# Performance work log

Measured on AMD Instinct MI355X. Metric: run time of the kernel, lower is better.

Reference implementation:

```python
import jax, jax.numpy as jnp
import numpy as np

N_NODES = 100000
N_EDGES = 1600000
N_GRAPHS = 256
IN_C = 64
HID = 128
OUT = 128
BN_EPS = 1e-5


def setup_inputs() -> dict:
    key = jax.random.key(0)
    ks = jax.random.split(key, 24)
    x = jax.random.normal(ks[0], (N_NODES, IN_C), jnp.float32)
    edge_index = jax.random.randint(ks[1], (2, N_EDGES), 0, N_NODES, dtype=jnp.int64 if jax.config.jax_enable_x64 else jnp.int32)
    batch = jnp.sort(jax.random.randint(ks[2], (N_NODES,), 0, N_GRAPHS))

    def lin(k, i, o):
        return (jax.random.normal(k, (i, o), jnp.float32) / np.float32(np.sqrt(i)))

    d = {"x": x, "edge_index": edge_index, "batch": batch}
    in_dims = [IN_C, HID, HID]
    for l in range(3):
        d[f"w1_{l}"] = lin(ks[3 + 6 * l], in_dims[l], HID)
        d[f"b1_{l}"] = jnp.zeros((HID,), jnp.float32)
        d[f"w2_{l}"] = lin(ks[4 + 6 * l], HID, HID)
        d[f"b2_{l}"] = jnp.zeros((HID,), jnp.float32)
        d[f"gamma_{l}"] = jnp.ones((HID,), jnp.float32)
        d[f"beta_{l}"] = jnp.zeros((HID,), jnp.float32)
    d["proj_w"] = lin(ks[22], HID, OUT)
    d["proj_b"] = jnp.zeros((OUT,), jnp.float32)
    return d


def _gin_forward(x, edge_index, batch, layers, proj_w, proj_b):
    src, dst = edge_index[0], edge_index[1]
    h = x
    for (w1, b1, w2, b2, g, b) in layers:
        # GINConv (eps=0, aggr='add'): MLP(h_i + sum_{j->i} h_j)
        agg = jax.ops.segment_sum(h[src], dst, num_segments=h.shape[0])
        z = h + agg
        z = jax.nn.relu(z @ w1 + b1) @ w2 + b2
        # BatchNorm1d, training mode (biased batch stats)
        mean = z.mean(axis=0)
        var = z.var(axis=0)
        z = (z - mean) * jax.lax.rsqrt(var + BN_EPS) * g + b
        h = jax.nn.relu(z)
    # global_mean_pool over graph ids
    s = jax.ops.segment_sum(h, batch, num_segments=N_GRAPHS)
    cnt = jax.ops.segment_sum(jnp.ones((h.shape[0], 1), h.dtype), batch, num_segments=N_GRAPHS)
    hg = s / jnp.maximum(cnt, 1.0)
    return hg @ proj_w + proj_b


def reference(x, edge_index, batch,
              w1_0, b1_0, w2_0, b2_0, gamma_0, beta_0,
              w1_1, b1_1, w2_1, b2_1, gamma_1, beta_1,
              w1_2, b1_2, w2_2, b2_2, gamma_2, beta_2,
              proj_w, proj_b):
    layers = [
        (w1_0, b1_0, w2_0, b2_0, gamma_0, beta_0),
        (w1_1, b1_1, w2_1, b2_1, gamma_1, beta_1),
        (w1_2, b1_2, w2_2, b2_2, gamma_2, beta_2),
    ]
    return _gin_forward(x, edge_index, batch, layers, proj_w, proj_b)
```

## Files before the change

### kernel.cpp

```cpp
#include <hip/hip_runtime.h>

#define N_NODES 100000
#define N_EDGES 1600000
#define N_GRAPHS 256
#define HID 128
#define BN_EPS 1e-5f

#define NT 1563
#define EB 4096
#define RB 391
#define MBLK 391
#define PB 1564

typedef __bf16 bf16x8 __attribute__((ext_vector_type(8)));
typedef __bf16 bf16x4 __attribute__((ext_vector_type(4)));
typedef __bf16 bf16x2 __attribute__((ext_vector_type(2)));
typedef float f32x4 __attribute__((ext_vector_type(4)));

__global__ __launch_bounds__(256) void setup_kernel(
    const float* __restrict__ x, __bf16* __restrict__ xb,
    const float* __restrict__ wa, const float* __restrict__ wb,
    const float* __restrict__ wc, const float* __restrict__ wd,
    const float* __restrict__ we, const float* __restrict__ wf,
    __bf16* __restrict__ wt,
    const int* __restrict__ batch, int* __restrict__ counts,
    const int* __restrict__ ei, int* __restrict__ tcnt) {
  __shared__ int hist[NT];
  int b = blockIdx.x;
  if (b < 6250) {
    int idx = b * 256 + threadIdx.x;
    if (idx >= N_NODES * 16) return;
    f32x4 v = ((const f32x4*)x)[idx];
    bf16x4 o = {(__bf16)v[0], (__bf16)v[1], (__bf16)v[2], (__bf16)v[3]};
    ((bf16x4*)xb)[idx] = o;
  } else if (b < 6250 + 352) {
    int idx = (b - 6250) * 256 + threadIdx.x;
    if (idx >= 90112) return;
    const float* w;
    int K, local;
    if (idx < 8192) { w = wa; K = 64; local = idx; }
    else {
      int s = (idx - 8192) / 16384;
      local = (idx - 8192) - s * 16384;
      K = 128;
      w = (s == 0) ? wb : (s == 1) ? wc : (s == 2) ? wd : (s == 3) ? we : wf;
    }
    int n = local / K, k = local - n * K;
    wt[idx] = (__bf16)w[k * 128 + n];
  } else if (b < 6609) {
    int t = (b - 6602) * 256 + threadIdx.x;
    int r0 = t * 64;
    if (r0 >= N_NODES) return;
    int rend = min(r0 + 64, N_NODES);
    int curg = batch[r0], cnt = 0;
    for (int r = r0; r < rend; r++) {
      int g = batch[r];
      if (g != curg) {
        atomicAdd(&counts[curg], cnt);
        curg = g;
        cnt = 1;
      } else {
        cnt++;
      }
    }
    atomicAdd(&counts[curg], cnt);
  } else {
    int t = threadIdx.x;
    for (int i = t; i < NT; i += 256) hist[i] = 0;
    __syncthreads();
    int base = (b - 6609) * EB;
#pragma unroll 4
    for (int i = 0; i < EB / 256; i++) {
      int e = base + i * 256 + t;
      if (e < N_EDGES) atomicAdd(&hist[ei[N_EDGES + e] >> 6], 1);
    }
    __syncthreads();
    for (int i = t; i < NT; i += 256) {
      int h = hist[i];
      if (h) atomicAdd(&tcnt[i], h);
    }
  }
}

__global__ __launch_bounds__(256) void tile_scan_kernel(const int* __restrict__ tcnt,
                                                        int* __restrict__ tstart,
                                                        int* __restrict__ gcursor) {
  __shared__ int ps[256];
  int t = threadIdx.x;
  const int CH = (NT + 255) / 256;
  int lo = t * CH, hi = min(lo + CH, NT);
  int s = 0;
  for (int i = lo; i < hi; i++) s += tcnt[i];
  ps[t] = s;
  __syncthreads();
  for (int off = 1; off < 256; off <<= 1) {
    int v = ps[t];
    int u = (t >= off) ? ps[t - off] : 0;
    __syncthreads();
    ps[t] = v + u;
    __syncthreads();
  }
  int base = (t == 0) ? 0 : ps[t - 1];
  for (int i = lo; i < hi; i++) {
    tstart[i] = base;
    gcursor[i] = base;
    base += tcnt[i];
  }
  if (t == 0) tstart[NT] = N_EDGES;
}

__global__ __launch_bounds__(256) void reorder2_kernel(const int* __restrict__ ei,
                                                       int* __restrict__ gcursor,
                                                       int* __restrict__ epack) {
  __shared__ int hist[NT];
  int t = threadIdx.x;
  for (int i = t; i < NT; i += 256) hist[i] = 0;
  __syncthreads();
  int base = blockIdx.x * EB;
#pragma unroll 4
  for (int i = 0; i < EB / 256; i++) {
    int e = base + i * 256 + t;
    if (e < N_EDGES) atomicAdd(&hist[ei[N_EDGES + e] >> 6], 1);
  }
  __syncthreads();
  for (int i = t; i < NT; i += 256) {
    int h = hist[i];
    if (h) hist[i] = atomicAdd(&gcursor[i], h);
  }
  __syncthreads();
#pragma unroll 4
  for (int i = 0; i < EB / 256; i++) {
    int e = base + i * 256 + t;
    if (e < N_EDGES) {
      int d = ei[N_EDGES + e];
      int s = ei[e];
      int pos = atomicAdd(&hist[d >> 6], 1);
      epack[pos] = (s << 6) | (d & 63);
    }
  }
}

__global__ __launch_bounds__(256) void row_sort_kernel(const int* __restrict__ tstart,
                                                       const int* __restrict__ epack,
                                                       int* __restrict__ starts,
                                                       int* __restrict__ srcs) {
  __shared__ int cnt[64];
  __shared__ int rbase[65];
  __shared__ int rofs[64];
  int t = threadIdx.x, b = blockIdx.x;
  int ts = tstart[b], te = tstart[b + 1];
  if (t < 64) cnt[t] = 0;
  __syncthreads();
  for (int i = ts + t; i < te; i += 256) atomicAdd(&cnt[epack[i] & 63], 1);
  __syncthreads();
  if (t == 0) {
    int a = 0;
    for (int r = 0; r < 64; r++) { rbase[r] = a; a += cnt[r]; }
    rbase[64] = a;
  }
  __syncthreads();
  if (t < 64) rofs[t] = ts + rbase[t];
  if (t <= 64) {
    int gr = b * 64 + t;
    if (gr <= N_NODES) starts[gr] = ts + rbase[t];
  }
  __syncthreads();
  for (int i = ts + t; i < te; i += 256) {
    int p = epack[i];
    int pos = atomicAdd(&rofs[p & 63], 1);
    srcs[pos] = p >> 6;
  }
}

template <int C, bool BN>
__global__ __launch_bounds__(256) void gather_kernel(const __bf16* __restrict__ h,
                                                     const float* __restrict__ accum,
                                                     const float* __restrict__ gamma,
                                                     const float* __restrict__ beta,
                                                     const int* __restrict__ starts,
                                                     const int* __restrict__ srcs,
                                                     __bf16* __restrict__ z) {
  const int lane = threadIdx.x & 63;
  const int row = __builtin_amdgcn_readfirstlane(blockIdx.x * 4 + (threadIdx.x >> 6));
  const int e0 = starts[row], e1 = starts[row + 1];

  if constexpr (C == 128) {
    float a0 = 0.f, a1 = 0.f, b0 = 0.f, b1 = 0.f;
    if constexpr (BN) {
      const int c0 = lane * 2, c1 = c0 + 1;
      const float invN = 1.f / (float)N_NODES;
      float m0 = accum[c0] * invN, m1 = accum[c1] * invN;
      float v0 = accum[HID + c0] * invN - m0 * m0;
      float v1 = accum[HID + c1] * invN - m1 * m1;
      a0 = gamma[c0] * rsqrtf(v0 + BN_EPS);
      a1 = gamma[c1] * rsqrtf(v1 + BN_EPS);
      b0 = beta[c0] - m0 * a0;
      b1 = beta[c1] - m1 * a1;
    }
#define ACCBN(vv, ss)                                                  \
    do {                                                               \
      if constexpr (BN) {                                              \
        ss.x += fmaxf(fmaf(a0, (float)(vv)[0], b0), 0.f);              \
        ss.y += fmaxf(fmaf(a1, (float)(vv)[1], b1), 0.f);              \
      } else {                                                         \
        ss.x += (float)(vv)[0];                                        \
        ss.y += (float)(vv)[1];                                        \
      }                                                                \
    } while (0)
    float2 s0 = {0.f, 0.f}, s1 = {0.f, 0.f}, s2 = {0.f, 0.f}, s3 = {0.f, 0.f};
    float2 s4 = {0.f, 0.f}, s5 = {0.f, 0.f}, s6 = {0.f, 0.f}, s7 = {0.f, 0.f};
    int e = e0;
    for (; e + 7 < e1; e += 8) {
      int i0 = srcs[e];
      int i1 = srcs[e + 1];
      int i2 = srcs[e + 2];
      int i3 = srcs[e + 3];
      int i4 = srcs[e + 4];
      int i5 = srcs[e + 5];
      int i6 = srcs[e + 6];
      int i7 = srcs[e + 7];
      bf16x2 v0 = *(const bf16x2*)(h + (size_t)i0 * 128 + lane * 2);
      bf16x2 v1 = *(const bf16x2*)(h + (size_t)i1 * 128 + lane * 2);
      bf16x2 v2 = *(const bf16x2*)(h + (size_t)i2 * 128 + lane * 2);
      bf16x2 v3 = *(const bf16x2*)(h + (size_t)i3 * 128 + lane * 2);
      bf16x2 v4 = *(const bf16x2*)(h + (size_t)i4 * 128 + lane * 2);
      bf16x2 v5 = *(const bf16x2*)(h + (size_t)i5 * 128 + lane * 2);
      bf16x2 v6 = *(const bf16x2*)(h + (size_t)i6 * 128 + lane * 2);
      bf16x2 v7 = *(const bf16x2*)(h + (size_t)i7 * 128 + lane * 2);
      ACCBN(v0, s0);
      ACCBN(v1, s1);
      ACCBN(v2, s2);
      ACCBN(v3, s3);
      ACCBN(v4, s4);
      ACCBN(v5, s5);
      ACCBN(v6, s6);
      ACCBN(v7, s7);
    }
    for (; e + 3 < e1; e += 4) {
      int i0 = srcs[e];
      int i1 = srcs[e + 1];
      int i2 = srcs[e + 2];
      int i3 = srcs[e + 3];
      bf16x2 v0 = *(const bf16x2*)(h + (size_t)i0 * 128 + lane * 2);
      bf16x2 v1 = *(const bf16x2*)(h + (size_t)i1 * 128 + lane * 2);
      bf16x2 v2 = *(const bf16x2*)(h + (size_t)i2 * 128 + lane * 2);
      bf16x2 v3 = *(const bf16x2*)(h + (size_t)i3 * 128 + lane * 2);
      ACCBN(v0, s0);
      ACCBN(v1, s1);
      ACCBN(v2, s2);
      ACCBN(v3, s3);
    }
    for (; e < e1; e++) {
      int i0 = srcs[e];
      bf16x2 vv = *(const bf16x2*)(h + (size_t)i0 * 128 + lane * 2);
      ACCBN(vv, s0);
    }
    bf16x2 sv = *(const bf16x2*)(h + (size_t)row * 128 + lane * 2);
    ACCBN(sv, s0);
    float tx = ((s0.x + s1.x) + (s2.x + s3.x)) + ((s4.x + s5.x) + (s6.x + s7.x));
    float ty = ((s0.y + s1.y) + (s2.y + s3.y)) + ((s4.y + s5.y) + (s6.y + s7.y));
    bf16x2 o = {(__bf16)tx, (__bf16)ty};
    *(bf16x2*)(z + (size_t)row * 128 + lane * 2) = o;
#undef ACCBN
  } else {
    float s0 = 0.f, s1 = 0.f, s2 = 0.f, s3 = 0.f;
    float s4 = 0.f, s5 = 0.f, s6 = 0.f, s7 = 0.f;
    int e = e0;
    for (; e + 7 < e1; e += 8) {
      int i0 = srcs[e];
      int i1 = srcs[e + 1];
      int i2 = srcs[e + 2];
      int i3 = srcs[e + 3];
      int i4 = srcs[e + 4];
      int i5 = srcs[e + 5];
      int i6 = srcs[e + 6];
      int i7 = srcs[e + 7];
      s0 += (float)h[(size_t)i0 * 64 + lane];
      s1 += (float)h[(size_t)i1 * 64 + lane];
      s2 += (float)h[(size_t)i2 * 64 + lane];
      s3 += (float)h[(size_t)i3 * 64 + lane];
      s4 += (float)h[(size_t)i4 * 64 + lane];
      s5 += (float)h[(size_t)i5 * 64 + lane];
      s6 += (float)h[(size_t)i6 * 64 + lane];
      s7 += (float)h[(size_t)i7 * 64 + lane];
    }
    for (; e + 3 < e1; e += 4) {
      int i0 = srcs[e];
      int i1 = srcs[e + 1];
      int i2 = srcs[e + 2];
      int i3 = srcs[e + 3];
      s0 += (float)h[(size_t)i0 * 64 + lane];
      s1 += (float)h[(size_t)i1 * 64 + lane];
      s2 += (float)h[(size_t)i2 * 64 + lane];
      s3 += (float)h[(size_t)i3 * 64 + lane];
    }
    for (; e < e1; e++) {
      int i0 = srcs[e];
      s0 += (float)h[(size_t)i0 * 64 + lane];
    }
    s0 += (float)h[(size_t)row * 64 + lane];
    float tot = ((s0 + s1) + (s2 + s3)) + ((s4 + s5) + (s6 + s7));
    z[(size_t)row * 64 + lane] = (__bf16)tot;
  }
}

template <int CIN>
__global__ __launch_bounds__(256, 1) void mlp_kernel(
    const __bf16* __restrict__ z, const __bf16* __restrict__ w1t,
    const float* __restrict__ b1, const __bf16* __restrict__ w2t,
    const float* __restrict__ b2, __bf16* __restrict__ u,
    float* __restrict__ part) {
  constexpr int CINP = CIN + 8;
  constexpr int TS = HID + 8;
  __shared__ __align__(16) __bf16 w1s[128 * CINP];
  __shared__ __align__(16) __bf16 w2s[128 * TS];
  __shared__ __align__(16) __bf16 hsm[4 * 64 * TS];

  const int tid = threadIdx.x;

  for (int i = tid; i < 128 * (CIN / 8); i += 256) {
    int r = i / (CIN / 8), c = i - r * (CIN / 8);
    *(bf16x8*)(w1s + r * CINP + c * 8) = *(const bf16x8*)(w1t + r * CIN + c * 8);
  }
  for (int i = tid; i < 128 * 16; i += 256) {
    int r = i >> 4, c = i & 15;
    *(bf16x8*)(w2s + r * TS + c * 8) = *(const bf16x8*)(w2t + r * HID + c * 8);
  }
  __syncthreads();

  const int wid = tid >> 6;
  const int lane = tid & 63;
  const int l16 = lane & 15;
  const int quad = lane >> 4;
  const int wgid = blockIdx.x * 4 + wid;
  const int rowbase = wgid * 64;
  const int nvalid = min(64, N_NODES - rowbase);
  __bf16* sm = hsm + wid * 64 * TS;

  if (nvalid <= 0) {
    float2 z2 = {0.f, 0.f};
    *(float2*)(part + (size_t)wgid * 256 + lane * 2) = z2;
    *(float2*)(part + (size_t)wgid * 256 + HID + lane * 2) = z2;
    return;
  }

  const f32x4 zero4 = {0.f, 0.f, 0.f, 0.f};
  f32x4 acc[8][4];

  {
#pragma unroll
    for (int ct = 0; ct < 8; ct++)
#pragma unroll
      for (int m = 0; m < 4; m++) acc[ct][m] = zero4;
#pragma unroll
    for (int ks = 0; ks < CIN / 32; ks++) {
      bf16x8 af[4];
#pragma unroll
      for (int m = 0; m < 4; m++) {
        int row = min(rowbase + m * 16 + l16, N_NODES - 1);
        af[m] = *(const bf16x8*)(z + (size_t)row * CIN + ks * 32 + quad * 8);
      }
#pragma unroll
      for (int ct = 0; ct < 8; ct++) {
        bf16x8 bfr = *(const bf16x8*)(w1s + (ct * 16 + l16) * CINP + ks * 32 + quad * 8);
#pragma unroll
        for (int m = 0; m < 4; m++)
          acc[ct][m] = __builtin_amdgcn_mfma_f32_16x16x32_bf16(af[m], bfr, acc[ct][m], 0, 0, 0);
      }
    }
#pragma unroll
    for (int ct = 0; ct < 8; ct++) {
      int col = ct * 16 + l16;
      float bias = b1[col];
#pragma unroll
      for (int m = 0; m < 4; m++)
#pragma unroll
        for (int r = 0; r < 4; r++) {
          float v = acc[ct][m][r] + bias;
          sm[(m * 16 + quad * 4 + r) * TS + col] = (__bf16)(v > 0.f ? v : 0.f);
        }
    }
  }

  {
#pragma unroll
    for (int ct = 0; ct < 8; ct++)
#pragma unroll
      for (int m = 0; m < 4; m++) acc[ct][m] = zero4;
#pragma unroll
    for (int ks = 0; ks < HID / 32; ks++) {
      bf16x8 af[4];
#pragma unroll
      for (int m = 0; m < 4; m++)
        af[m] = *(const bf16x8*)(sm + (m * 16 + l16) * TS + ks * 32 + quad * 8);
#pragma unroll
      for (int ct = 0; ct < 8; ct++) {
        bf16x8 bfr = *(const bf16x8*)(w2s + (ct * 16 + l16) * TS + ks * 32 + quad * 8);
#pragma unroll
        for (int m = 0; m < 4; m++)
          acc[ct][m] = __builtin_amdgcn_mfma_f32_16x16x32_bf16(af[m], bfr, acc[ct][m], 0, 0, 0);
      }
    }
  }

#pragma unroll
  for (int ct = 0; ct < 8; ct++) {
    int col = ct * 16 + l16;
    float bias = b2[col];
#pragma unroll
    for (int m = 0; m < 4; m++)
#pragma unroll
      for (int r = 0; r < 4; r++)
        sm[(m * 16 + quad * 4 + r) * TS + col] = (__bf16)(acc[ct][m][r] + bias);
  }

  for (int f = lane; f < nvalid * 16; f += 64) {
    int r = f >> 4, c8 = f & 15;
    bf16x8 v = *(const bf16x8*)(sm + r * TS + c8 * 8);
    *(bf16x8*)(u + (size_t)(rowbase + r) * HID + c8 * 8) = v;
  }

  {
    float s0 = 0.f, q0 = 0.f, s1 = 0.f, q1 = 0.f;
    for (int r = 0; r < nvalid; r++) {
      bf16x2 v = *(const bf16x2*)(sm + r * TS + lane * 2);
      float f0 = (float)v[0], f1 = (float)v[1];
      s0 += f0; q0 += f0 * f0;
      s1 += f1; q1 += f1 * f1;
    }
    float2 sp = {s0, s1}, qp = {q0, q1};
    *(float2*)(part + (size_t)wgid * 256 + lane * 2) = sp;
    *(float2*)(part + (size_t)wgid * 256 + HID + lane * 2) = qp;
  }
}

__global__ __launch_bounds__(256) void reduce_part_kernel(const float* __restrict__ part,
                                                          float* __restrict__ accum) {
  int t = threadIdx.x;
  float s = 0.f;
  for (int r = blockIdx.x; r < PB; r += gridDim.x)
    s += part[(size_t)r * 256 + t];
  atomicAdd(&accum[t], s);
}

__global__ __launch_bounds__(128) void bn_apply_pool_kernel(const __bf16* __restrict__ u,
                                                            const float* __restrict__ accum,
                                                            const float* __restrict__ gamma,
                                                            const float* __restrict__ beta,
                                                            const int* __restrict__ batch,
                                                            float* __restrict__ pool) {
  int c = threadIdx.x;
  int r0 = blockIdx.x * 64;
  if (r0 >= N_NODES) return;
  int rend = min(r0 + 64, N_NODES);
  const float invN = 1.f / (float)N_NODES;
  float mean = accum[c] * invN;
  float var = accum[HID + c] * invN - mean * mean;
  float a = gamma[c] * rsqrtf(var + BN_EPS);
  float b = beta[c] - mean * a;
  float accv = 0.f;
  int curg = -1;
  for (int r = r0; r < rend; r++) {
    int g = batch[r];
    if (g != curg) {
      if (curg >= 0) atomicAdd(&pool[curg * HID + c], accv);
      curg = g;
      accv = 0.f;
    }
    float v = (float)u[(size_t)r * HID + c];
    v = v * a + b;
    accv += (v > 0.f ? v : 0.f);
  }
  if (curg >= 0) atomicAdd(&pool[curg * HID + c], accv);
}

__global__ __launch_bounds__(128) void pool_proj_kernel(const float* __restrict__ pool,
                                                        const int* __restrict__ counts,
                                                        const float* __restrict__ pw,
                                                        const float* __restrict__ pb,
                                                        float* __restrict__ out) {
  int g = blockIdx.x;
  int c = threadIdx.x;
  __shared__ float hg[HID];
  float cnt = (float)max(counts[g], 1);
  hg[c] = pool[g * HID + c] / cnt;
  __syncthreads();
  float acc = pb[c];
#pragma unroll 8
  for (int k = 0; k < HID; k++) acc += hg[k] * pw[k * HID + c];
  out[g * HID + c] = acc;
}

extern "C" void kernel_launch(void* const* d_in, const int* in_sizes, int n_in,
                              void* d_out, int out_size, void* d_ws, size_t ws_size,
                              hipStream_t stream) {
  (void)in_sizes; (void)n_in; (void)out_size; (void)ws_size;
  const float* x = (const float*)d_in[0];
  const int* ei = (const int*)d_in[1];
  const int* batch = (const int*)d_in[2];
  const float* w1[3] = {(const float*)d_in[3], (const float*)d_in[9], (const float*)d_in[15]};
  const float* b1[3] = {(const float*)d_in[4], (const float*)d_in[10], (const float*)d_in[16]};
  const float* w2[3] = {(const float*)d_in[5], (const float*)d_in[11], (const float*)d_in[17]};
  const float* b2[3] = {(const float*)d_in[6], (const float*)d_in[12], (const float*)d_in[18]};
  const float* gm[3] = {(const float*)d_in[7], (const float*)d_in[13], (const float*)d_in[19]};
  const float* bt[3] = {(const float*)d_in[8], (const float*)d_in[14], (const float*)d_in[20]};
  const float* pw = (const float*)d_in[21];
  const float* pb = (const float*)d_in[22];
  float* out = (float*)d_out;

  char* ws = (char*)d_ws;
  __bf16* bufA = (__bf16*)ws;        ws += (size_t)N_NODES * HID * 2;
  __bf16* bufB = (__bf16*)ws;        ws += (size_t)N_NODES * HID * 2;
  __bf16* bufC = (__bf16*)ws;        ws += (size_t)N_NODES * HID * 2;
  __bf16* z0 = (__bf16*)ws;          ws += (size_t)N_NODES * 64 * 2;
  __bf16* xb = (__bf16*)ws;          ws += (size_t)N_NODES * 64 * 2;
  int* srcs = (int*)ws;              ws += (size_t)N_EDGES * 4;
  int* epack = (int*)ws;             ws += (size_t)N_EDGES * 4;
  int* starts = (int*)ws;            ws += (size_t)(N_NODES + 1) * 4;
  int* tcnt = (int*)ws;              ws += NT * 4;
  int* tstart = (int*)ws;            ws += (NT + 1) * 4;
  int* gcursor = (int*)ws;           ws += NT * 4;
  ws = (char*)(((uintptr_t)ws + 63) & ~(uintptr_t)63);
  float* part = (float*)ws;          ws += (size_t)PB * 256 * 4;
  __bf16* wt_all = (__bf16*)ws;      ws += 90112 * 2;
  ws = (char*)(((uintptr_t)ws + 63) & ~(uintptr_t)63);
  float* accum = (float*)ws;         ws += 3 * 256 * 4;
  float* pool = (float*)ws;          ws += N_GRAPHS * HID * 4;
  int* counts = (int*)ws;            ws += N_GRAPHS * 4;

  __bf16* w1t0 = wt_all;
  __bf16* w2t0 = wt_all + 8192;
  __bf16* w1t1 = wt_all + 24576;
  __bf16* w2t1 = wt_all + 40960;
  __bf16* w1t2 = wt_all + 57344;
  __bf16* w2t2 = wt_all + 73728;

  float* acc0 = accum;
  float* acc1 = accum + 256;
  float* acc2 = accum + 512;

  const int gat_blocks = (N_NODES + 3) / 4;

  hipMemsetAsync(accum, 0, 3 * 256 * 4 + (size_t)N_GRAPHS * HID * 4 + N_GRAPHS * 4, stream);
  hipMemsetAsync(tcnt, 0, NT * 4, stream);

  setup_kernel<<<7000, 256, 0, stream>>>(x, xb, w1[0], w2[0], w1[1], w2[1],
                                         w1[2], w2[2], wt_all, batch, counts, ei, tcnt);

  tile_scan_kernel<<<1, 256, 0, stream>>>(tcnt, tstart, gcursor);
  reorder2_kernel<<<RB, 256, 0, stream>>>(ei, gcursor, epack);
  row_sort_kernel<<<NT, 256, 0, stream>>>(tstart, epack, starts, srcs);

  gather_kernel<64, false><<<gat_blocks, 256, 0, stream>>>(xb, nullptr, nullptr, nullptr,
                                                           starts, srcs, z0);
  mlp_kernel<64><<<MBLK, 256, 0, stream>>>(z0, w1t0, b1[0], w2t0, b2[0], bufA, part);
  reduce_part_kernel<<<128, 256, 0, stream>>>(part, acc0);

  gather_kernel<128, true><<<gat_blocks, 256, 0, stream>>>(bufA, acc0, gm[0], bt[0],
                                                           starts, srcs, bufC);
  mlp_kernel<128><<<MBLK, 256, 0, stream>>>(bufC, w1t1, b1[1], w2t1, b2[1], bufB, part);
  reduce_part_kernel<<<128, 256, 0, stream>>>(part, acc1);

  gather_kernel<128, true><<<gat_blocks, 256, 0, stream>>>(bufB, acc1, gm[1], bt[1],
                                                           starts, srcs, bufC);
  mlp_kernel<128><<<MBLK, 256, 0, stream>>>(bufC, w1t2, b1[2], w2t2, b2[2], bufA, part);
  reduce_part_kernel<<<128, 256, 0, stream>>>(part, acc2);

  bn_apply_pool_kernel<<<NT, 128, 0, stream>>>(bufA, acc2, gm[2], bt[2], batch, pool);

  pool_proj_kernel<<<N_GRAPHS, 128, 0, stream>>>(pool, counts, pw, pb, out);
}
```

Measured before the change: 490.2 us.

## Restructure MLP kernel to 8 waves of 32 rows with per-16-row sub-tiles

The MLP kernel now launches 512 threads (8 waves), each wave handling 32 rows processed as two sequential 16-row sub-tiles instead of one 64-row tile. Accumulator state drops from 32 to 8 MFMA tiles per wave and the shared staging buffer shrinks accordingly. The partial-stats buffer doubles to match the larger number of waves. This is meant to lower register pressure and raise parallelism per CU, but each loaded weight fragment now feeds fewer MFMAs, so there is less reuse of the B operand.

```diff
diff --git a/kernel.cpp b/kernel.cpp
--- a/kernel.cpp
+++ b/kernel.cpp
@@ -10,7 +10,7 @@
 #define EB 4096
 #define RB 391
 #define MBLK 391
-#define PB 1564
+#define PB 3128
 
 typedef __bf16 bf16x8 __attribute__((ext_vector_type(8)));
 typedef __bf16 bf16x4 __attribute__((ext_vector_type(4)));
@@ -305,7 +305,7 @@
 }
 
 template <int CIN>
-__global__ __launch_bounds__(256, 1) void mlp_kernel(
+__global__ __launch_bounds__(512, 1) void mlp_kernel(
     const __bf16* __restrict__ z, const __bf16* __restrict__ w1t,
     const float* __restrict__ b1, const __bf16* __restrict__ w2t,
     const float* __restrict__ b2, __bf16* __restrict__ u,
@@ -314,15 +314,15 @@
   constexpr int TS = HID + 8;
   __shared__ __align__(16) __bf16 w1s[128 * CINP];
   __shared__ __align__(16) __bf16 w2s[128 * TS];
-  __shared__ __align__(16) __bf16 hsm[4 * 64 * TS];
+  __shared__ __align__(16) __bf16 hsm[8 * 16 * TS];
 
   const int tid = threadIdx.x;
 
-  for (int i = tid; i < 128 * (CIN / 8); i += 256) {
+  for (int i = tid; i < 128 * (CIN / 8); i += 512) {
     int r = i / (CIN / 8), c = i - r * (CIN / 8);
     *(bf16x8*)(w1s + r * CINP + c * 8) = *(const bf16x8*)(w1t + r * CIN + c * 8);
   }
-  for (int i = tid; i < 128 * 16; i += 256) {
+  for (int i = tid; i < 128 * 16; i += 512) {
     int r = i >> 4, c = i & 15;
     *(bf16x8*)(w2s + r * TS + c * 8) = *(const bf16x8*)(w2t + r * HID + c * 8);
   }
@@ -332,10 +332,10 @@
   const int lane = tid & 63;
   const int l16 = lane & 15;
   const int quad = lane >> 4;
-  const int wgid = blockIdx.x * 4 + wid;
-  const int rowbase = wgid * 64;
-  const int nvalid = min(64, N_NODES - rowbase);
-  __bf16* sm = hsm + wid * 64 * TS;
+  const int wgid = blockIdx.x * 8 + wid;
+  const int rowbase = wgid * 32;
+  const int nvalid = min(32, N_NODES - rowbase);
+  __bf16* sm = hsm + wid * 16 * TS;
 
   if (nvalid <= 0) {
     float2 z2 = {0.f, 0.f};
@@ -345,27 +345,24 @@
   }
 
   const f32x4 zero4 = {0.f, 0.f, 0.f, 0.f};
-  f32x4 acc[8][4];
-
-  {
-#pragma unroll
-    for (int ct = 0; ct < 8; ct++)
-#pragma unroll
-      for (int m = 0; m < 4; m++) acc[ct][m] = zero4;
+  float s0 = 0.f, q0 = 0.f, s1 = 0.f, q1 = 0.f;
+
+#pragma unroll
+  for (int m = 0; m < 2; m++) {
+    const int mbase = rowbase + m * 16;
+    const int nv_m = min(16, max(0, nvalid - m * 16));
+
+    f32x4 acc[8];
+#pragma unroll
+    for (int ct = 0; ct < 8; ct++) acc[ct] = zero4;
 #pragma unroll
     for (int ks = 0; ks < CIN / 32; ks++) {
-      bf16x8 af[4];
-#pragma unroll
-      for (int m = 0; m < 4; m++) {
-        int row = min(rowbase + m * 16 + l16, N_NODES - 1);
-        af[m] = *(const bf16x8*)(z + (size_t)row * CIN + ks * 32 + quad * 8);
-      }
+      bf16x8 af = *(const bf16x8*)(z + (size_t)min(mbase + l16, N_NODES - 1) * CIN +
+                                   ks * 32 + quad * 8);
 #pragma unroll
       for (int ct = 0; ct < 8; ct++) {
         bf16x8 bfr = *(const bf16x8*)(w1s + (ct * 16 + l16) * CINP + ks * 32 + quad * 8);
-#pragma unroll
-        for (int m = 0; m < 4; m++)
-          acc[ct][m] = __builtin_amdgcn_mfma_f32_16x16x32_bf16(af[m], bfr, acc[ct][m], 0, 0, 0);
+        acc[ct] = __builtin_amdgcn_mfma_f32_16x16x32_bf16(af, bfr, acc[ct], 0, 0, 0);
       }
     }
 #pragma unroll
@@ -373,61 +370,48 @@
       int col = ct * 16 + l16;
       float bias = b1[col];
 #pragma unroll
-      for (int m = 0; m < 4; m++)
-#pragma unroll
-        for (int r = 0; r < 4; r++) {
-          float v = acc[ct][m][r] + bias;
-          sm[(m * 16 + quad * 4 + r) * TS + col] = (__bf16)(v > 0.f ? v : 0.f);
-        }
-    }
-  }
-
-  {
-#pragma unroll
-    for (int ct = 0; ct < 8; ct++)
-#pragma unroll
-      for (int m = 0; m < 4; m++) acc[ct][m] = zero4;
+      for (int r = 0; r < 4; r++) {
+        float v = acc[ct][r] + bias;
+        sm[(quad * 4 + r) * TS + col] = (__bf16)(v > 0.f ? v : 0.f);
+      }
+    }
+
+#pragma unroll
+    for (int ct = 0; ct < 8; ct++) acc[ct] = zero4;
 #pragma unroll
     for (int ks = 0; ks < HID / 32; ks++) {
-      bf16x8 af[4];
-#pragma unroll
-      for (int m = 0; m < 4; m++)
-        af[m] = *(const bf16x8*)(sm + (m * 16 + l16) * TS + ks * 32 + quad * 8);
+      bf16x8 af = *(const bf16x8*)(sm + l16 * TS + ks * 32 + quad * 8);
 #pragma unroll
       for (int ct = 0; ct < 8; ct++) {
         bf16x8 bfr = *(const bf16x8*)(w2s + (ct * 16 + l16) * TS + ks * 32 + quad * 8);
-#pragma unroll
-        for (int m = 0; m < 4; m++)
-          acc[ct][m] = __builtin_amdgcn_mfma_f32_16x16x32_bf16(af[m], bfr, acc[ct][m], 0, 0, 0);
+        acc[ct] = __builtin_amdgcn_mfma_f32_16x16x32_bf16(af, bfr, acc[ct], 0, 0, 0);
       }
     }
-  }
-
-#pragma unroll
-  for (int ct = 0; ct < 8; ct++) {
-    int col = ct * 16 + l16;
-    float bias = b2[col];
-#pragma unroll
-    for (int m = 0; m < 4; m++)
+
+#pragma unroll
+    for (int ct = 0; ct < 8; ct++) {
+      int col = ct * 16 + l16;
+      float bias = b2[col];
 #pragma unroll
       for (int r = 0; r < 4; r++)
-        sm[(m * 16 + quad * 4 + r) * TS + col] = (__bf16)(acc[ct][m][r] + bias);
-  }
-
-  for (int f = lane; f < nvalid * 16; f += 64) {
-    int r = f >> 4, c8 = f & 15;
-    bf16x8 v = *(const bf16x8*)(sm + r * TS + c8 * 8);
-    *(bf16x8*)(u + (size_t)(rowbase + r) * HID + c8 * 8) = v;
-  }
-
-  {
-    float s0 = 0.f, q0 = 0.f, s1 = 0.f, q1 = 0.f;
-    for (int r = 0; r < nvalid; r++) {
+        sm[(quad * 4 + r) * TS + col] = (__bf16)(acc[ct][r] + bias);
+    }
+
+    for (int f = lane; f < nv_m * 16; f += 64) {
+      int r = f >> 4, c8 = f & 15;
+      bf16x8 v = *(const bf16x8*)(sm + r * TS + c8 * 8);
+      *(bf16x8*)(u + (size_t)(mbase + r) * HID + c8 * 8) = v;
+    }
+
+    for (int r = 0; r < nv_m; r++) {
       bf16x2 v = *(const bf16x2*)(sm + r * TS + lane * 2);
       float f0 = (float)v[0], f1 = (float)v[1];
       s0 += f0; q0 += f0 * f0;
       s1 += f1; q1 += f1 * f1;
     }
+  }
+
+  {
     float2 sp = {s0, s1}, qp = {q0, q1};
     *(float2*)(part + (size_t)wgid * 256 + lane * 2) = sp;
     *(float2*)(part + (size_t)wgid * 256 + HID + lane * 2) = qp;
@@ -553,17 +537,17 @@
 
   gather_kernel<64, false><<<gat_blocks, 256, 0, stream>>>(xb, nullptr, nullptr, nullptr,
                                                            starts, srcs, z0);
-  mlp_kernel<64><<<MBLK, 256, 0, stream>>>(z0, w1t0, b1[0], w2t0, b2[0], bufA, part);
+  mlp_kernel<64><<<MBLK, 512, 0, stream>>>(z0, w1t0, b1[0], w2t0, b2[0], bufA, part);
   reduce_part_kernel<<<128, 256, 0, stream>>>(part, acc0);
 
   gather_kernel<128, true><<<gat_blocks, 256, 0, stream>>>(bufA, acc0, gm[0], bt[0],
                                                            starts, srcs, bufC);
-  mlp_kernel<128><<<MBLK, 256, 0, stream>>>(bufC, w1t1, b1[1], w2t1, b2[1], bufB, part);
+  mlp_kernel<128><<<MBLK, 512, 0, stream>>>(bufC, w1t1, b1[1], w2t1, b2[1], bufB, part);
   reduce_part_kernel<<<128, 256, 0, stream>>>(part, acc1);
 
   gather_kernel<128, true><<<gat_blocks, 256, 0, stream>>>(bufB, acc1, gm[1], bt[1],
                                                            starts, srcs, bufC);
-  mlp_kernel<128><<<MBLK, 256, 0, stream>>>(bufC, w1t2, b1[2], w2t2, b2[2], bufA, part);
+  mlp_kernel<128><<<MBLK, 512, 0, stream>>>(bufC, w1t2, b1[2], w2t2, b2[2], bufA, part);
   reduce_part_kernel<<<128, 256, 0, stream>>>(part, acc2);
 
   bn_apply_pool_kernel<<<NT, 128, 0, stream>>>(bufA, acc2, gm[2], bt[2], batch, pool);
```

Result: no change. 490.7 us (+0.1%).
